# Performance work log

Hardware: AMD Instinct MI355X
Metric: run time of the kernel (lower is better)

## Reference

```python
import jax, jax.numpy as jnp
import numpy as np

B, D, U, E, K = 4096, 1024, 1024, 8, 2


def setup_inputs() -> dict:
    key = jax.random.key(0)
    ks = jax.random.split(key, 5)
    lim_e = np.sqrt(6.0 / D)  # he_uniform-style fan_in scaling per expert
    return {
        "x": jax.random.normal(ks[0], (B, D), dtype=jnp.float32),
        "expert_mu": jax.random.uniform(ks[1], (D, U, E), jnp.float32, -lim_e, lim_e),
        "expert_rho": -2.6 + 0.01 * jax.random.normal(ks[2], (U, E), dtype=jnp.float32),
        "expert_bias": jnp.zeros((U, E), dtype=jnp.float32),
        "gating_kernel": jax.random.uniform(ks[3], (D, E), jnp.float32, -lim_e, lim_e),
        "gating_bias": jnp.zeros((E,), dtype=jnp.float32),
        "eps": jax.random.normal(ks[4], (U, E), dtype=jnp.float32),
        "k": K,
    }


def reference(x, expert_mu, expert_rho, expert_bias, gating_kernel, gating_bias, eps, k):
    # --- gating: softmax over experts, keep top-k, renormalize ---
    logits = x @ gating_kernel + gating_bias            # [B, E]
    gates = jax.nn.softmax(logits, axis=-1)             # [B, E]
    top_vals, top_idx = jax.lax.top_k(gates, k)         # [B, k]
    mask = jnp.zeros_like(gates).at[jnp.arange(x.shape[0])[:, None], top_idx].set(1.0)
    gw = gates * mask
    gw = gw / jnp.sum(gw, axis=-1, keepdims=True)       # renormalized top-k gates [B, E]

    # --- Bayesian experts: W_e = mu_e + softplus(rho_e)*eps_e (eps shared over data dim) ---
    # x @ (sigma*eps broadcast over d) == sum_d(x_d) * sigma*eps  (exact)
    sigma = jax.nn.softplus(expert_rho)                 # [U, E]
    mean_out = jnp.einsum('bd,due->bue', x, expert_mu)  # [B, U, E]
    noise_out = jnp.sum(x, axis=-1)[:, None, None] * (sigma * eps)[None]  # [B, U, E]
    expert_out = mean_out + noise_out + expert_bias[None]                 # linear expert_activation

    # --- gate-weighted combination ---
    y = jnp.einsum('bue,be->bu', expert_out, gw)        # [B, U]
    return y
```

## Files before the change

kernel.cpp:

```cpp
#include <hip/hip_runtime.h>
#include <hip/hip_bf16.h>

typedef unsigned short u16;
typedef __attribute__((ext_vector_type(8))) short bf16x8;
typedef __attribute__((ext_vector_type(4))) float f32x4;

#define BDIM 4096
#define DDIM 1024
#define UDIM 1024
#define NE 8
#define NDIM 8192
#define NPAIR 28
#define PL_CAP 4160
#define MAX_MT 92

__device__ __forceinline__ u16 f2bf(float f) {
    unsigned int u = __float_as_uint(f);
    u += 0x7fffu + ((u >> 16) & 1u);
    return (u16)(u >> 16);
}

__device__ __forceinline__ void gload_lds16(const u16* g, u16* lds) {
    __builtin_amdgcn_global_load_lds(
        (const __attribute__((address_space(1))) void*)g,
        (__attribute__((address_space(3))) void*)lds, 16, 0, 0);
}

__global__ __launch_bounds__(256) void prep_kernel(
    const float* __restrict__ mu, const float* __restrict__ x,
    const float* __restrict__ gk, const float* __restrict__ gb,
    const float* __restrict__ rho, const float* __restrict__ eps,
    u16* __restrict__ Wt, u16* __restrict__ xb,
    float* __restrict__ xsum, int4* __restrict__ pkb,
    float* __restrict__ se)
{
    __shared__ u16 tile[64 * 68];
    const int bx = blockIdx.x;
    const int tid = threadIdx.x;

    if (bx < 2048) {
        const int n0 = (bx & 127) << 6;
        const int d0 = (bx >> 7) << 6;
        const int nq = (tid & 15) << 2;
        const int dr = tid >> 4;
#pragma unroll
        for (int p = 0; p < 4; ++p) {
            int dl = p * 16 + dr;
            float4 v = *(const float4*)&mu[(size_t)(d0 + dl) * NDIM + n0 + nq];
            ushort4 o;
            o.x = f2bf(v.x); o.y = f2bf(v.y); o.z = f2bf(v.z); o.w = f2bf(v.w);
            *(uint2*)&tile[dl * 68 + nq] = *(uint2*)&o;
        }
        __syncthreads();
#pragma unroll
        for (int issue = 0; issue < 2; ++issue) {
            int nloc = issue * 32 + (tid >> 3);
            int d8 = (tid & 7) * 8;
            uint4 o; u16* tp = (u16*)&o;
#pragma unroll
            for (int i = 0; i < 8; ++i) tp[i] = tile[(d8 + i) * 68 + nloc];
            *(uint4*)&Wt[(size_t)(n0 + nloc) * DDIM + d0 + d8] = o;
        }
    } else if (bx < 3072) {
        const int b = (bx - 2048) * 4 + (tid >> 6);
        const int lane = tid & 63;
        float acc[8] = {0.f,0.f,0.f,0.f,0.f,0.f,0.f,0.f};
        float xs = 0.f;
        const float4* x4 = (const float4*)&x[(size_t)b * DDIM];
        ushort4* xb4 = (ushort4*)&xb[(size_t)b * DDIM];
#pragma unroll
        for (int it = 0; it < 4; ++it) {
            int i4 = it * 64 + lane;
            float4 v = x4[i4];
            ushort4 o;
            o.x = f2bf(v.x); o.y = f2bf(v.y); o.z = f2bf(v.z); o.w = f2bf(v.w);
            xb4[i4] = o;
            xs += v.x + v.y + v.z + v.w;
            const float4* g4 = (const float4*)&gk[(size_t)i4 * 4 * NE];
#pragma unroll
            for (int j = 0; j < 4; ++j) {
                float xv = ((const float*)&v)[j];
                float4 ga = g4[j * 2], gc = g4[j * 2 + 1];
                acc[0] += xv * ga.x; acc[1] += xv * ga.y; acc[2] += xv * ga.z; acc[3] += xv * ga.w;
                acc[4] += xv * gc.x; acc[5] += xv * gc.y; acc[6] += xv * gc.z; acc[7] += xv * gc.w;
            }
        }
#pragma unroll
        for (int off = 32; off >= 1; off >>= 1) {
            xs += __shfl_xor(xs, off);
#pragma unroll
            for (int e = 0; e < 8; ++e) acc[e] += __shfl_xor(acc[e], off);
        }
        if (lane == 0) {
            float lg[8];
#pragma unroll
            for (int e = 0; e < 8; ++e) lg[e] = acc[e] + gb[e];
            int i1 = 0;
#pragma unroll
            for (int e = 1; e < 8; ++e) if (lg[e] > lg[i1]) i1 = e;
            int i2 = (i1 == 0) ? 1 : 0;
#pragma unroll
            for (int e = 0; e < 8; ++e) {
                if (e == i1 || e == i2) continue;
                if (lg[e] > lg[i2]) i2 = e;
            }
            float p1 = 1.f / (1.f + expf(lg[i2] - lg[i1]));
            float p2 = 1.f - p1;
            xsum[b] = xs;
            pkb[b] = make_int4(i1, i2, __float_as_int(p1), __float_as_int(p2));
        }
    } else {
        int i = (bx - 3072) * 256 + tid;
        float r = rho[i];
        se[i] = log1pf(expf(r)) * eps[i];
    }
}

__global__ __launch_bounds__(256) void pairlist_kernel(
    const int4* __restrict__ pkb, int* __restrict__ cnt,
    u16* __restrict__ plist)
{
    const int pid = blockIdx.x;
    int p = 0, rem = pid;
    while (rem >= 7 - p) { rem -= 7 - p; ++p; }
    const int q = p + 1 + rem;

    const int tid = threadIdx.x;
    const int wv = tid >> 6, lane = tid & 63;
    __shared__ int wsum[4];
    __shared__ int sbase;
    if (tid == 0) sbase = 0;
    __syncthreads();
    u16* pl = plist + pid * PL_CAP;
    for (int chunk = 0; chunk < BDIM; chunk += 256) {
        int b = chunk + tid;
        int4 pk = pkb[b];
        int lo = min(pk.x, pk.y), hi = max(pk.x, pk.y);
        bool f = (lo == p) && (hi == q);
        unsigned long long m = __ballot(f);
        int prefix = __popcll(m & ((1ULL << lane) - 1ULL));
        if (lane == 0) wsum[wv] = __popcll(m);
        __syncthreads();
        int wbase = sbase;
        for (int w = 0; w < wv; ++w) wbase += wsum[w];
        if (f) pl[wbase + prefix] = (u16)b;
        __syncthreads();
        if (tid == 0) sbase += wsum[0] + wsum[1] + wsum[2] + wsum[3];
        __syncthreads();
    }
    int c = sbase;
    int pc = (c + 63) & ~63;
    for (int i = c + tid; i < pc; i += 256) pl[i] = (u16)0xFFFF;
    if (tid == 0) cnt[pid] = c;
}

__global__ __launch_bounds__(256, 3) void gemm_pair_kernel(
    const u16* __restrict__ Xb,
    const u16* __restrict__ Wt,
    const int4* __restrict__ pkb,
    const float* __restrict__ xsum,
    const float* __restrict__ se,
    const float* __restrict__ biasv,
    const int* __restrict__ cnt,
    const u16* __restrict__ plist,
    float* __restrict__ y)
{
    const int bid = blockIdx.x;
    const int ntile = bid & 15;
    const int t = bid >> 4;
    int pid = 0, base = 0;
    for (; pid < NPAIR; ++pid) {
        int mt = (cnt[pid] + 63) >> 6;
        if (t < base + mt) break;
        base += mt;
    }
    if (pid >= NPAIR) return;
    const int m0 = (t - base) << 6;
    int p = 0, rem = pid;
    while (rem >= 7 - p) { rem -= 7 - p; ++p; }
    const int q = p + 1 + rem;
    const int u0 = ntile << 6;

    __shared__ u16 As[2][64 * 64];
    __shared__ u16 Bp[2][64 * 64];
    __shared__ u16 Bq[2][64 * 64];

    const int tid  = threadIdx.x;
    const int lane = tid & 63;
    const int wid  = tid >> 6;
    const int wm = wid >> 1, wn = wid & 1;
    const int l15 = lane & 15;
    const int l4  = lane >> 4;

    const u16* __restrict__ rowl = plist + pid * PL_CAP + m0;
    const int stg_off = tid * 8;
    const int sc = (((tid & 7) ^ ((tid >> 3) & 7))) * 8;

    const u16* aP[2];
    const u16* bpP[2];
    const u16* bqP[2];
#pragma unroll
    for (int it = 0; it < 2; ++it) {
        int r = it * 32 + (tid >> 3);
        int rid = rowl[r];
        if (rid == 0xFFFF) rid = 0;
        aP[it]  = Xb + (size_t)rid * DDIM + sc;
        bpP[it] = Wt + ((size_t)(u0 + r) * NE + p) * DDIM + sc;
        bqP[it] = Wt + ((size_t)(u0 + r) * NE + q) * DDIM + sc;
    }

#define STAGE(BUF, KK) do {                                     \
        gload_lds16(aP[0]  + (KK), &As[BUF][stg_off]);          \
        gload_lds16(aP[1]  + (KK), &As[BUF][2048 + stg_off]);   \
        gload_lds16(bpP[0] + (KK), &Bp[BUF][stg_off]);          \
        gload_lds16(bpP[1] + (KK), &Bp[BUF][2048 + stg_off]);   \
        gload_lds16(bqP[0] + (KK), &Bq[BUF][stg_off]);          \
        gload_lds16(bqP[1] + (KK), &Bq[BUF][2048 + stg_off]);   \
    } while (0)

    f32x4 accp[2][2] = {};
    f32x4 accq[2][2] = {};

    STAGE(0, 0);
    STAGE(1, 64);

    const int sw = l15 & 7;

#pragma unroll
    for (int t2 = 0; t2 < 16; ++t2) {
        const int cur = t2 & 1;
        if (t2 < 15) asm volatile("s_waitcnt vmcnt(6)" ::: "memory");
        else         asm volatile("s_waitcnt vmcnt(0)" ::: "memory");
        __builtin_amdgcn_s_barrier();
        __builtin_amdgcn_sched_barrier(0);
#pragma unroll
        for (int k2 = 0; k2 < 2; ++k2) {
            const int cx = ((k2 * 4 + l4) ^ sw) * 8;
            bf16x8 av[2], bpv[2], bqv[2];
#pragma unroll
            for (int m = 0; m < 2; ++m)
                av[m] = *(const bf16x8*)&As[cur][(wm * 32 + m * 16 + l15) * 64 + cx];
#pragma unroll
            for (int n = 0; n < 2; ++n) {
                bpv[n] = *(const bf16x8*)&Bp[cur][(wn * 32 + n * 16 + l15) * 64 + cx];
                bqv[n] = *(const bf16x8*)&Bq[cur][(wn * 32 + n * 16 + l15) * 64 + cx];
            }
#pragma unroll
            for (int m = 0; m < 2; ++m)
#pragma unroll
                for (int n = 0; n < 2; ++n) {
                    accp[m][n] = __builtin_amdgcn_mfma_f32_16x16x32_bf16(av[m], bpv[n], accp[m][n], 0, 0, 0);
                    accq[m][n] = __builtin_amdgcn_mfma_f32_16x16x32_bf16(av[m], bqv[n], accq[m][n], 0, 0, 0);
                }
        }
        __builtin_amdgcn_sched_barrier(0);
        __builtin_amdgcn_s_barrier();
        if (t2 < 14) STAGE(cur, (t2 + 2) * 64);
    }
#undef STAGE

    float sep_[2], seq_[2], bip_[2], biq_[2];
#pragma unroll
    for (int n = 0; n < 2; ++n) {
        int u = u0 + wn * 32 + n * 16 + l15;
        sep_[n] = se[u * NE + p];    seq_[n] = se[u * NE + q];
        bip_[n] = biasv[u * NE + p]; biq_[n] = biasv[u * NE + q];
    }
#pragma unroll
    for (int m = 0; m < 2; ++m) {
#pragma unroll
        for (int jj = 0; jj < 4; ++jj) {
            int r_loc = wm * 32 + m * 16 + l4 * 4 + jj;
            u16 b16 = rowl[r_loc];
            if (b16 == (u16)0xFFFF) continue;
            int b = (int)b16;
            int4 pk = pkb[b];
            float wp, wq;
            if (pk.x == p) { wp = __int_as_float(pk.z); wq = __int_as_float(pk.w); }
            else           { wp = __int_as_float(pk.w); wq = __int_as_float(pk.z); }
            float xs = xsum[b];
            float* yrow = &y[(size_t)b * UDIM];
#pragma unroll
            for (int n = 0; n < 2; ++n) {
                int u = u0 + wn * 32 + n * 16 + l15;
                float val = wp * (accp[m][n][jj] + xs * sep_[n] + bip_[n])
                          + wq * (accq[m][n][jj] + xs * seq_[n] + biq_[n]);
                yrow[u] = val;
            }
        }
    }
}

extern "C" void kernel_launch(void* const* d_in, const int* in_sizes, int n_in,
                              void* d_out, int out_size, void* d_ws, size_t ws_size,
                              hipStream_t stream) {
    const float* x    = (const float*)d_in[0];
    const float* mu   = (const float*)d_in[1];
    const float* rho  = (const float*)d_in[2];
    const float* bias = (const float*)d_in[3];
    const float* gk   = (const float*)d_in[4];
    const float* gb   = (const float*)d_in[5];
    const float* eps  = (const float*)d_in[6];
    float* y = (float*)d_out;

    char* ws = (char*)d_ws;
    u16*   Wt   = (u16*)ws;
    u16*   xb   = (u16*)(ws + 16777216);
    float* xsp  = (float*)(ws + 25165824);
    float* sep  = (float*)(ws + 25182208);
    int*   cnt  = (int*)(ws + 25214976);
    int4*  pkb  = (int4*)(ws + 25215104);
    u16*   prl  = (u16*)(ws + 25280640);
    if (ws_size < 25513600) return;

    prep_kernel<<<dim3(3104), dim3(256), 0, stream>>>(
        mu, x, gk, gb, rho, eps, Wt, xb, xsp, pkb, sep);
    pairlist_kernel<<<dim3(NPAIR), dim3(256), 0, stream>>>(pkb, cnt, prl);
    gemm_pair_kernel<<<dim3(MAX_MT * 16), dim3(256), 0, stream>>>(
        xb, Wt, pkb, xsp, sep, bias, cnt, prl, y);
}
```

Before: 87.42 us.

## Widen GEMM tile to 128 columns with 512 threads and split-K across wave halves

```diff
diff --git a/kernel.cpp b/kernel.cpp
--- a/kernel.cpp
+++ b/kernel.cpp
@@ -154,7 +154,7 @@
     if (tid == 0) cnt[pid] = c;
 }
 
-__global__ __launch_bounds__(256, 3) void gemm_pair_kernel(
+__global__ __launch_bounds__(512, 4) void gemm_pair_kernel(
     const u16* __restrict__ Xb,
     const u16* __restrict__ Wt,
     const int4* __restrict__ pkb,
@@ -166,8 +166,8 @@
     float* __restrict__ y)
 {
     const int bid = blockIdx.x;
-    const int ntile = bid & 15;
-    const int t = bid >> 4;
+    const int ntile = bid & 7;
+    const int t = bid >> 3;
     int pid = 0, base = 0;
     for (; pid < NPAIR; ++pid) {
         int mt = (cnt[pid] + 63) >> 6;
@@ -179,113 +179,138 @@
     int p = 0, rem = pid;
     while (rem >= 7 - p) { rem -= 7 - p; ++p; }
     const int q = p + 1 + rem;
-    const int u0 = ntile << 6;
-
-    __shared__ u16 As[2][64 * 64];
-    __shared__ u16 Bp[2][64 * 64];
-    __shared__ u16 Bq[2][64 * 64];
+    const int u0 = ntile << 7;
+
+    __shared__ u16 smem[40960];
+    u16* AsB = smem;
+    u16* BpB = smem + 8192;
+    u16* BqB = smem + 24576;
 
     const int tid  = threadIdx.x;
     const int lane = tid & 63;
     const int wid  = tid >> 6;
-    const int wm = wid >> 1, wn = wid & 1;
-    const int l15 = lane & 15;
-    const int l4  = lane >> 4;
+    const int h    = wid >> 2;
+    const int wn2  = (wid >> 1) & 1;
+    const int ew   = wid & 1;
+    const int l15  = lane & 15;
+    const int l4   = lane >> 4;
 
     const u16* __restrict__ rowl = plist + pid * PL_CAP + m0;
+    const int srow    = tid >> 3;
     const int stg_off = tid * 8;
-    const int sc = (((tid & 7) ^ ((tid >> 3) & 7))) * 8;
-
-    const u16* aP[2];
-    const u16* bpP[2];
-    const u16* bqP[2];
-#pragma unroll
-    for (int it = 0; it < 2; ++it) {
-        int r = it * 32 + (tid >> 3);
-        int rid = rowl[r];
-        if (rid == 0xFFFF) rid = 0;
-        aP[it]  = Xb + (size_t)rid * DDIM + sc;
-        bpP[it] = Wt + ((size_t)(u0 + r) * NE + p) * DDIM + sc;
-        bqP[it] = Wt + ((size_t)(u0 + r) * NE + q) * DDIM + sc;
-    }
-
-#define STAGE(BUF, KK) do {                                     \
-        gload_lds16(aP[0]  + (KK), &As[BUF][stg_off]);          \
-        gload_lds16(aP[1]  + (KK), &As[BUF][2048 + stg_off]);   \
-        gload_lds16(bpP[0] + (KK), &Bp[BUF][stg_off]);          \
-        gload_lds16(bpP[1] + (KK), &Bp[BUF][2048 + stg_off]);   \
-        gload_lds16(bqP[0] + (KK), &Bq[BUF][stg_off]);          \
-        gload_lds16(bqP[1] + (KK), &Bq[BUF][2048 + stg_off]);   \
+    const int sc = ((tid & 7) ^ (srow & 7)) * 8;
+
+    int rid = rowl[srow];
+    if (rid == 0xFFFF) rid = 0;
+    const u16* aP   = Xb + (size_t)rid * DDIM + sc;
+    const u16* bpP0 = Wt + ((size_t)(u0 + srow) * NE + p) * DDIM + sc;
+    const u16* bpP1 = Wt + ((size_t)(u0 + 64 + srow) * NE + p) * DDIM + sc;
+    const u16* bqP0 = Wt + ((size_t)(u0 + srow) * NE + q) * DDIM + sc;
+    const u16* bqP1 = Wt + ((size_t)(u0 + 64 + srow) * NE + q) * DDIM + sc;
+
+#define STAGE(BUF, KK) do {                                          \
+        gload_lds16(aP   + (KK), AsB + (BUF) * 4096 + stg_off);      \
+        gload_lds16(bpP0 + (KK), BpB + (BUF) * 8192 + stg_off);      \
+        gload_lds16(bpP1 + (KK), BpB + (BUF) * 8192 + 4096 + stg_off); \
+        gload_lds16(bqP0 + (KK), BqB + (BUF) * 8192 + stg_off);      \
+        gload_lds16(bqP1 + (KK), BqB + (BUF) * 8192 + 4096 + stg_off); \
     } while (0)
 
-    f32x4 accp[2][2] = {};
-    f32x4 accq[2][2] = {};
+#define MF(A, B, C) __builtin_amdgcn_mfma_f32_16x16x32_bf16((A), (B), (C), 0, 0, 0)
+
+    f32x4 acc[4][4] = {};
 
     STAGE(0, 0);
     STAGE(1, 64);
 
     const int sw = l15 & 7;
+    const int cx = ((h * 4 + l4) ^ sw) * 8;
+    const u16* Bsel = ew ? BqB : BpB;
 
 #pragma unroll
     for (int t2 = 0; t2 < 16; ++t2) {
         const int cur = t2 & 1;
-        if (t2 < 15) asm volatile("s_waitcnt vmcnt(6)" ::: "memory");
+        if (t2 < 15) asm volatile("s_waitcnt vmcnt(5)" ::: "memory");
         else         asm volatile("s_waitcnt vmcnt(0)" ::: "memory");
         __builtin_amdgcn_s_barrier();
         __builtin_amdgcn_sched_barrier(0);
-#pragma unroll
-        for (int k2 = 0; k2 < 2; ++k2) {
-            const int cx = ((k2 * 4 + l4) ^ sw) * 8;
-            bf16x8 av[2], bpv[2], bqv[2];
-#pragma unroll
-            for (int m = 0; m < 2; ++m)
-                av[m] = *(const bf16x8*)&As[cur][(wm * 32 + m * 16 + l15) * 64 + cx];
-#pragma unroll
-            for (int n = 0; n < 2; ++n) {
-                bpv[n] = *(const bf16x8*)&Bp[cur][(wn * 32 + n * 16 + l15) * 64 + cx];
-                bqv[n] = *(const bf16x8*)&Bq[cur][(wn * 32 + n * 16 + l15) * 64 + cx];
-            }
-#pragma unroll
-            for (int m = 0; m < 2; ++m)
-#pragma unroll
-                for (int n = 0; n < 2; ++n) {
-                    accp[m][n] = __builtin_amdgcn_mfma_f32_16x16x32_bf16(av[m], bpv[n], accp[m][n], 0, 0, 0);
-                    accq[m][n] = __builtin_amdgcn_mfma_f32_16x16x32_bf16(av[m], bqv[n], accq[m][n], 0, 0, 0);
-                }
-        }
+        const u16* Acur = AsB + cur * 4096;
+        const u16* Bcur = Bsel + cur * 8192 + wn2 * 4096;
+        bf16x8 av[4], bv[4];
+#pragma unroll
+        for (int m = 0; m < 4; ++m)
+            av[m] = *(const bf16x8*)&Acur[(m * 16 + l15) * 64 + cx];
+#pragma unroll
+        for (int n = 0; n < 4; ++n)
+            bv[n] = *(const bf16x8*)&Bcur[(n * 16 + l15) * 64 + cx];
+        __builtin_amdgcn_s_setprio(1);
+#pragma unroll
+        for (int m = 0; m < 4; ++m)
+#pragma unroll
+            for (int n = 0; n < 4; ++n)
+                acc[m][n] = MF(av[m], bv[n], acc[m][n]);
+        __builtin_amdgcn_s_setprio(0);
         __builtin_amdgcn_sched_barrier(0);
         __builtin_amdgcn_s_barrier();
         if (t2 < 14) STAGE(cur, (t2 + 2) * 64);
     }
 #undef STAGE
-
-    float sep_[2], seq_[2], bip_[2], biq_[2];
-#pragma unroll
-    for (int n = 0; n < 2; ++n) {
-        int u = u0 + wn * 32 + n * 16 + l15;
-        sep_[n] = se[u * NE + p];    seq_[n] = se[u * NE + q];
-        bip_[n] = biasv[u * NE + p]; biq_[n] = biasv[u * NE + q];
-    }
-#pragma unroll
-    for (int m = 0; m < 2; ++m) {
-#pragma unroll
-        for (int jj = 0; jj < 4; ++jj) {
-            int r_loc = wm * 32 + m * 16 + l4 * 4 + jj;
-            u16 b16 = rowl[r_loc];
-            if (b16 == (u16)0xFFFF) continue;
-            int b = (int)b16;
-            int4 pk = pkb[b];
-            float wp, wq;
-            if (pk.x == p) { wp = __int_as_float(pk.z); wq = __int_as_float(pk.w); }
-            else           { wp = __int_as_float(pk.w); wq = __int_as_float(pk.z); }
-            float xs = xsum[b];
-            float* yrow = &y[(size_t)b * UDIM];
-#pragma unroll
-            for (int n = 0; n < 2; ++n) {
-                int u = u0 + wn * 32 + n * 16 + l15;
-                float val = wp * (accp[m][n][jj] + xs * sep_[n] + bip_[n])
-                          + wq * (accq[m][n][jj] + xs * seq_[n] + biq_[n]);
-                yrow[u] = val;
+#undef MF
+
+    float* fb = (float*)smem;
+    const int FBE = 128 * 68;
+
+    if (h == 1) {
+#pragma unroll
+        for (int m = 0; m < 4; ++m)
+#pragma unroll
+            for (int n = 0; n < 4; ++n)
+                *(f32x4*)&fb[ew * FBE + (wn2 * 64 + n * 16 + l15) * 68 + (m * 16 + l4 * 4)] = acc[m][n];
+    }
+    __syncthreads();
+    if (h == 0) {
+#pragma unroll
+        for (int m = 0; m < 4; ++m)
+#pragma unroll
+            for (int n = 0; n < 4; ++n) {
+                f32x4* ptr = (f32x4*)&fb[ew * FBE + (wn2 * 64 + n * 16 + l15) * 68 + (m * 16 + l4 * 4)];
+                f32x4 v = *ptr;
+                v += acc[m][n];
+                *ptr = v;
+            }
+    }
+    __syncthreads();
+
+    float sepv[2], seqv[2], bipv[2], biqv[2];
+#pragma unroll
+    for (int ch = 0; ch < 2; ++ch) {
+        int u = u0 + ch * 64 + lane;
+        sepv[ch] = se[u * NE + p];    seqv[ch] = se[u * NE + q];
+        bipv[ch] = biasv[u * NE + p]; biqv[ch] = biasv[u * NE + q];
+    }
+    const int r0w = wid * 8;
+#pragma unroll
+    for (int rg = 0; rg < 2; ++rg) {
+        int rbase = r0w + rg * 4;
+#pragma unroll
+        for (int ch = 0; ch < 2; ++ch) {
+            int col = ch * 64 + lane;
+            f32x4 pa = *(const f32x4*)&fb[0 * FBE + col * 68 + rbase];
+            f32x4 qa = *(const f32x4*)&fb[1 * FBE + col * 68 + rbase];
+#pragma unroll
+            for (int j = 0; j < 4; ++j) {
+                int r_loc = rbase + j;
+                u16 b16 = rowl[r_loc];
+                if (b16 == (u16)0xFFFF) continue;
+                int b = (int)b16;
+                int4 pk = pkb[b];
+                float wp, wq;
+                if (pk.x == p) { wp = __int_as_float(pk.z); wq = __int_as_float(pk.w); }
+                else           { wp = __int_as_float(pk.w); wq = __int_as_float(pk.z); }
+                float xs = xsum[b];
+                float val = wp * (pa[j] + xs * sepv[ch] + bipv[ch])
+                          + wq * (qa[j] + xs * seqv[ch] + biqv[ch]);
+                y[(size_t)b * UDIM + u0 + col] = val;
             }
         }
     }
@@ -316,6 +341,6 @@
     prep_kernel<<<dim3(3104), dim3(256), 0, stream>>>(
         mu, x, gk, gb, rho, eps, Wt, xb, xsp, pkb, sep);
     pairlist_kernel<<<dim3(NPAIR), dim3(256), 0, stream>>>(pkb, cnt, prl);
-    gemm_pair_kernel<<<dim3(MAX_MT * 16), dim3(256), 0, stream>>>(
+    gemm_pair_kernel<<<dim3(MAX_MT * 8), dim3(512), 0, stream>>>(
         xb, Wt, pkb, xsp, sep, bias, cnt, prl, y);
 }
```

After: 95.22 us. 8.9% more time.

## Fuse pair-list construction into GEMM kernel, dropping separate pairlist launch

Applied to the files above, without the earlier changes.

```diff
diff --git a/kernel.cpp b/kernel.cpp
--- a/kernel.cpp
+++ b/kernel.cpp
@@ -11,7 +11,6 @@
 #define NE 8
 #define NDIM 8192
 #define NPAIR 28
-#define PL_CAP 4160
 #define MAX_MT 92
 
 __device__ __forceinline__ u16 f2bf(float f) {
@@ -116,44 +115,6 @@
     }
 }
 
-__global__ __launch_bounds__(256) void pairlist_kernel(
-    const int4* __restrict__ pkb, int* __restrict__ cnt,
-    u16* __restrict__ plist)
-{
-    const int pid = blockIdx.x;
-    int p = 0, rem = pid;
-    while (rem >= 7 - p) { rem -= 7 - p; ++p; }
-    const int q = p + 1 + rem;
-
-    const int tid = threadIdx.x;
-    const int wv = tid >> 6, lane = tid & 63;
-    __shared__ int wsum[4];
-    __shared__ int sbase;
-    if (tid == 0) sbase = 0;
-    __syncthreads();
-    u16* pl = plist + pid * PL_CAP;
-    for (int chunk = 0; chunk < BDIM; chunk += 256) {
-        int b = chunk + tid;
-        int4 pk = pkb[b];
-        int lo = min(pk.x, pk.y), hi = max(pk.x, pk.y);
-        bool f = (lo == p) && (hi == q);
-        unsigned long long m = __ballot(f);
-        int prefix = __popcll(m & ((1ULL << lane) - 1ULL));
-        if (lane == 0) wsum[wv] = __popcll(m);
-        __syncthreads();
-        int wbase = sbase;
-        for (int w = 0; w < wv; ++w) wbase += wsum[w];
-        if (f) pl[wbase + prefix] = (u16)b;
-        __syncthreads();
-        if (tid == 0) sbase += wsum[0] + wsum[1] + wsum[2] + wsum[3];
-        __syncthreads();
-    }
-    int c = sbase;
-    int pc = (c + 63) & ~63;
-    for (int i = c + tid; i < pc; i += 256) pl[i] = (u16)0xFFFF;
-    if (tid == 0) cnt[pid] = c;
-}
-
 __global__ __launch_bounds__(256, 3) void gemm_pair_kernel(
     const u16* __restrict__ Xb,
     const u16* __restrict__ Wt,
@@ -161,38 +122,84 @@
     const float* __restrict__ xsum,
     const float* __restrict__ se,
     const float* __restrict__ biasv,
-    const int* __restrict__ cnt,
-    const u16* __restrict__ plist,
     float* __restrict__ y)
 {
     const int bid = blockIdx.x;
     const int ntile = bid & 15;
     const int t = bid >> 4;
-    int pid = 0, base = 0;
-    for (; pid < NPAIR; ++pid) {
-        int mt = (cnt[pid] + 63) >> 6;
-        if (t < base + mt) break;
-        base += mt;
-    }
-    if (pid >= NPAIR) return;
-    const int m0 = (t - base) << 6;
+
+    const int tid  = threadIdx.x;
+    const int lane = tid & 63;
+    const int wid  = tid >> 6;
+    const int wv   = wid;
+
+    __shared__ int hcnt[NPAIR];
+    __shared__ int pbase[NPAIR + 1];
+    __shared__ int s_pid, s_m0;
+    __shared__ int wsum[4];
+    __shared__ int sbase_s;
+    __shared__ u16 rowl_s[64];
+
+    if (tid < NPAIR) hcnt[tid] = 0;
+    if (tid < 64) rowl_s[tid] = (u16)0xFFFF;
+    if (tid == 0) sbase_s = 0;
+    __syncthreads();
+#pragma unroll
+    for (int it = 0; it < 16; ++it) {
+        int b = it * 256 + tid;
+        int4 pk = pkb[b];
+        int lo = min(pk.x, pk.y), hi = max(pk.x, pk.y);
+        int pidb = lo * 7 - ((lo * (lo - 1)) >> 1) + (hi - lo - 1);
+        atomicAdd(&hcnt[pidb], 1);
+    }
+    __syncthreads();
+    if (tid == 0) {
+        pbase[0] = 0;
+        for (int pp = 0; pp < NPAIR; ++pp) pbase[pp + 1] = pbase[pp] + ((hcnt[pp] + 63) >> 6);
+        int pp = 0;
+        if (t < pbase[NPAIR]) { while (t >= pbase[pp + 1]) ++pp; }
+        s_pid = (t < pbase[NPAIR]) ? pp : -1;
+        s_m0  = (t < pbase[NPAIR]) ? ((t - pbase[pp]) << 6) : 0;
+    }
+    __syncthreads();
+    const int pid = s_pid;
+    if (pid < 0) return;
+    const int m0 = s_m0;
     int p = 0, rem = pid;
     while (rem >= 7 - p) { rem -= 7 - p; ++p; }
     const int q = p + 1 + rem;
     const int u0 = ntile << 6;
 
+    for (int chunk = 0; chunk < BDIM; chunk += 256) {
+        int b = chunk + tid;
+        int4 pk = pkb[b];
+        int lo = min(pk.x, pk.y), hi = max(pk.x, pk.y);
+        bool f = (lo == p) && (hi == q);
+        unsigned long long mm = __ballot(f);
+        int prefix = __popcll(mm & ((1ULL << lane) - 1ULL));
+        if (lane == 0) wsum[wv] = __popcll(mm);
+        __syncthreads();
+        int wbase = sbase_s;
+        for (int w = 0; w < wv; ++w) wbase += wsum[w];
+        if (f) {
+            int pos = wbase + prefix - m0;
+            if (pos >= 0 && pos < 64) rowl_s[pos] = (u16)b;
+        }
+        __syncthreads();
+        if (tid == 0) sbase_s += wsum[0] + wsum[1] + wsum[2] + wsum[3];
+        __syncthreads();
+        if (sbase_s >= m0 + 64) break;
+    }
+    __syncthreads();
+
     __shared__ u16 As[2][64 * 64];
     __shared__ u16 Bp[2][64 * 64];
     __shared__ u16 Bq[2][64 * 64];
 
-    const int tid  = threadIdx.x;
-    const int lane = tid & 63;
-    const int wid  = tid >> 6;
     const int wm = wid >> 1, wn = wid & 1;
     const int l15 = lane & 15;
     const int l4  = lane >> 4;
 
-    const u16* __restrict__ rowl = plist + pid * PL_CAP + m0;
     const int stg_off = tid * 8;
     const int sc = (((tid & 7) ^ ((tid >> 3) & 7))) * 8;
 
@@ -202,7 +209,7 @@
 #pragma unroll
     for (int it = 0; it < 2; ++it) {
         int r = it * 32 + (tid >> 3);
-        int rid = rowl[r];
+        int rid = rowl_s[r];
         if (rid == 0xFFFF) rid = 0;
         aP[it]  = Xb + (size_t)rid * DDIM + sc;
         bpP[it] = Wt + ((size_t)(u0 + r) * NE + p) * DDIM + sc;
@@ -271,7 +278,7 @@
 #pragma unroll
         for (int jj = 0; jj < 4; ++jj) {
             int r_loc = wm * 32 + m * 16 + l4 * 4 + jj;
-            u16 b16 = rowl[r_loc];
+            u16 b16 = rowl_s[r_loc];
             if (b16 == (u16)0xFFFF) continue;
             int b = (int)b16;
             int4 pk = pkb[b];
@@ -308,14 +315,11 @@
     u16*   xb   = (u16*)(ws + 16777216);
     float* xsp  = (float*)(ws + 25165824);
     float* sep  = (float*)(ws + 25182208);
-    int*   cnt  = (int*)(ws + 25214976);
-    int4*  pkb  = (int4*)(ws + 25215104);
-    u16*   prl  = (u16*)(ws + 25280640);
-    if (ws_size < 25513600) return;
+    int4*  pkb  = (int4*)(ws + 25214976);
+    if (ws_size < 25280512) return;
 
     prep_kernel<<<dim3(3104), dim3(256), 0, stream>>>(
         mu, x, gk, gb, rho, eps, Wt, xb, xsp, pkb, sep);
-    pairlist_kernel<<<dim3(NPAIR), dim3(256), 0, stream>>>(pkb, cnt, prl);
     gemm_pair_kernel<<<dim3(MAX_MT * 16), dim3(256), 0, stream>>>(
-        xb, Wt, pkb, xsp, sep, bias, cnt, prl, y);
-}
+        xb, Wt, pkb, xsp, sep, bias, y);
+}
```

Result: slower. 97.35 us (+11.4%).
